# Kernel tuning notes

Measured on AMD Instinct MI355X. Metric: run time of the kernel, lower is better.

The kernel has to match this reference:

```python
import jax, jax.numpy as jnp
import numpy as np

# 'linear' blur taps from the source module
_KERNEL_1D = np.array([1/8, 3/8, 3/8, 1/8], dtype=np.float32)


def setup_inputs() -> dict:
    key = jax.random.key(0)
    B, C, H, W = 8, 256, 256, 256
    x = jax.random.normal(key, (B, C, H, W), dtype=jnp.float32)
    # 2D separable blur kernel: outer product of the 1D taps (registered buffer)
    kernel = jnp.asarray(np.outer(_KERNEL_1D, _KERNEL_1D))  # [4, 4]
    return {"x": x, "kernel": kernel}


def reference(x, kernel):
    # pad = k//2 - 1 = 1, reflect padding (torch 'reflect' == numpy 'reflect')
    pad = kernel.shape[0] // 2 - 1
    xp = jnp.pad(x, ((0, 0), (0, 0), (pad, pad), (pad, pad)), mode="reflect")
    C = x.shape[1]
    # Original builds a C x C weight that is zero off-diagonal; math is exactly a
    # depthwise (per-channel) conv with the same 4x4 blur kernel, stride 2.
    w = jnp.broadcast_to(kernel, (C, 1) + kernel.shape)  # [C, 1, 4, 4]
    out = jax.lax.conv_general_dilated(
        xp, w,
        window_strides=(2, 2),
        padding="VALID",
        dimension_numbers=("NCHW", "OIHW", "NCHW"),
        feature_group_count=C,
    )
    return out
```

## Files before the change

kernel.cpp:

```cpp
#include <hip/hip_runtime.h>


#define K0 0.125f
#define K1 0.375f

__global__ __launch_bounds__(256) void downsample2d_kernel(
    const float* __restrict__ x, float* __restrict__ out)
{
    const int tid         = threadIdx.x;
    const int lane_w      = tid & 31;
    const int pair_in_blk = tid >> 5;
    const int blk         = blockIdx.x & 7;
    const int plane       = blockIdx.x >> 3;

    const int ow4  = lane_w << 2;
    const int pair = blk * 8 + pair_in_blk;
    const int oh0  = pair * 2;
    const int ir_base = 2 * oh0 - 1;

    const float* xp = x   + (size_t)plane * (256 * 256);
    float*       op = out + (size_t)plane * (128 * 128);

    const int c_mid = ow4 * 2;
    const int cl = (ow4 == 0)   ? 1   : c_mid - 1;
    const int cr = (ow4 == 124) ? 254 : c_mid + 8;

    float acc0[4] = {0.f, 0.f, 0.f, 0.f};
    float acc1[4] = {0.f, 0.f, 0.f, 0.f};
    const float kv[4] = {K0, K1, K1, K0};

    #pragma unroll
    for (int r = 0; r < 6; ++r) {
        int ir = ir_base + r;
        ir = (ir < 0) ? 1 : ((ir > 255) ? 254 : ir);
        const float* row = xp + ir * 256;

        float  v0 = row[cl];
        float4 a  = *(const float4*)(row + c_mid);
        float4 b  = *(const float4*)(row + c_mid + 4);
        float  v9 = row[cr];

        float h0 = K0*v0  + K1*a.x + K1*a.y + K0*a.z;
        float h1 = K0*a.y + K1*a.z + K1*a.w + K0*b.x;
        float h2 = K0*a.w + K1*b.x + K1*b.y + K0*b.z;
        float h3 = K0*b.y + K1*b.z + K1*b.w + K0*v9;

        if (r < 4) {
            float w = kv[r];
            acc0[0] += w*h0; acc0[1] += w*h1; acc0[2] += w*h2; acc0[3] += w*h3;
        }
        if (r >= 2) {
            float w = kv[r - 2];
            acc1[0] += w*h0; acc1[1] += w*h1; acc1[2] += w*h2; acc1[3] += w*h3;
        }
    }

    *(float4*)(op + (size_t)oh0       * 128 + ow4) =
        make_float4(acc0[0], acc0[1], acc0[2], acc0[3]);
    *(float4*)(op + (size_t)(oh0 + 1) * 128 + ow4) =
        make_float4(acc1[0], acc1[1], acc1[2], acc1[3]);
}

extern "C" void kernel_launch(void* const* d_in, const int* in_sizes, int n_in,
                              void* d_out, int out_size, void* d_ws, size_t ws_size,
                              hipStream_t stream) {
    const float* x = (const float*)d_in[0];
    float* out = (float*)d_out;

    const int planes = 8 * 256;
    const int blocks = planes * 8;
    downsample2d_kernel<<<blocks, 256, 0, stream>>>(x, out);
}
```

Before: 721.5 us.

## Stage 34-row input strip in LDS and slide vertical window per thread

Each block now loads a 34x256 strip of the input plane into shared memory with coalesced float4 loads, then each thread computes one output column over 8 rows, reusing horizontally-filtered rows across a sliding window. This removes the redundant global reads of overlapping rows (previously 6 rows per 2 outputs) and unaligned edge scalar loads. It adds a 34KB LDS allocation per block, which limits occupancy, a barrier, and scalar strided LDS reads with stride-2 patterns that may cause bank conflicts.

```diff
diff --git a/kernel.cpp b/kernel.cpp
--- a/kernel.cpp
+++ b/kernel.cpp
@@ -4,61 +4,61 @@
 #define K0 0.125f
 #define K1 0.375f
 
-__global__ __launch_bounds__(256) void downsample2d_kernel(
+__global__ __launch_bounds__(256, 4) void downsample2d_kernel(
     const float* __restrict__ x, float* __restrict__ out)
 {
-    const int tid         = threadIdx.x;
-    const int lane_w      = tid & 31;
-    const int pair_in_blk = tid >> 5;
-    const int blk         = blockIdx.x & 7;
-    const int plane       = blockIdx.x >> 3;
+    __shared__ float lds[34 * 256];
 
-    const int ow4  = lane_w << 2;
-    const int pair = blk * 8 + pair_in_blk;
-    const int oh0  = pair * 2;
-    const int ir_base = 2 * oh0 - 1;
+    const int tid   = threadIdx.x;
+    const int strip = blockIdx.x & 7;
+    const int plane = blockIdx.x >> 3;
+    const int oh0   = strip * 16;
+    const int ir0   = 2 * oh0 - 1;
 
-    const float* xp = x   + (size_t)plane * (256 * 256);
-    float*       op = out + (size_t)plane * (128 * 128);
+    const float* xp = x + (size_t)plane * (256 * 256);
 
-    const int c_mid = ow4 * 2;
-    const int cl = (ow4 == 0)   ? 1   : c_mid - 1;
-    const int cr = (ow4 == 124) ? 254 : c_mid + 8;
-
-    float acc0[4] = {0.f, 0.f, 0.f, 0.f};
-    float acc1[4] = {0.f, 0.f, 0.f, 0.f};
-    const float kv[4] = {K0, K1, K1, K0};
-
+    const int lin0 = tid << 2;
     #pragma unroll
-    for (int r = 0; r < 6; ++r) {
-        int ir = ir_base + r;
-        ir = (ir < 0) ? 1 : ((ir > 255) ? 254 : ir);
-        const float* row = xp + ir * 256;
-
-        float  v0 = row[cl];
-        float4 a  = *(const float4*)(row + c_mid);
-        float4 b  = *(const float4*)(row + c_mid + 4);
-        float  v9 = row[cr];
-
-        float h0 = K0*v0  + K1*a.x + K1*a.y + K0*a.z;
-        float h1 = K0*a.y + K1*a.z + K1*a.w + K0*b.x;
-        float h2 = K0*a.w + K1*b.x + K1*b.y + K0*b.z;
-        float h3 = K0*b.y + K1*b.z + K1*b.w + K0*v9;
-
-        if (r < 4) {
-            float w = kv[r];
-            acc0[0] += w*h0; acc0[1] += w*h1; acc0[2] += w*h2; acc0[3] += w*h3;
-        }
-        if (r >= 2) {
-            float w = kv[r - 2];
-            acc1[0] += w*h0; acc1[1] += w*h1; acc1[2] += w*h2; acc1[3] += w*h3;
+    for (int i = 0; i < 9; ++i) {
+        int linear = i * 1024 + lin0;
+        int r = linear >> 8;
+        if (r < 34) {
+            int c  = linear & 255;
+            int gr = ir0 + r;
+            gr = (gr < 0) ? 1 : ((gr > 255) ? 254 : gr);
+            float4 v = *(const float4*)(xp + gr * 256 + c);
+            *(float4*)(&lds[linear]) = v;
         }
     }
+    __syncthreads();
 
-    *(float4*)(op + (size_t)oh0       * 128 + ow4) =
-        make_float4(acc0[0], acc0[1], acc0[2], acc0[3]);
-    *(float4*)(op + (size_t)(oh0 + 1) * 128 + ow4) =
-        make_float4(acc1[0], acc1[1], acc1[2], acc1[3]);
+    const int ow   = tid & 127;
+    const int half = tid >> 7;
+    const float* L = lds + (half << 4) * 256;
+
+    const int c1 = 2 * ow;
+    const float* pm = L + ((ow == 0)   ? 1   : c1 - 1);
+    const float* p0 = L + c1;
+    const float* pp = L + ((ow == 127) ? 254 : c1 + 2);
+
+    auto H = [&](int lr) {
+        int o = lr * 256;
+        return K0 * pm[o] + K1 * p0[o] + K1 * p0[o + 1] + K0 * pp[o];
+    };
+
+    float* op = out + (size_t)plane * (128 * 128)
+                    + (size_t)(oh0 + (half << 3)) * 128 + ow;
+
+    float h0 = H(0);
+    float h1 = H(1);
+    #pragma unroll
+    for (int l = 0; l < 8; ++l) {
+        float h2 = H(2 * l + 2);
+        float h3 = H(2 * l + 3);
+        op[l * 128] = K0 * h0 + K1 * h1 + K1 * h2 + K0 * h3;
+        h0 = h2;
+        h1 = h3;
+    }
 }
 
 extern "C" void kernel_launch(void* const* d_in, const int* in_sizes, int n_in,
```

Result: no change. 707.5 us (-1.9%).
